# Optimization experiments

Hardware: AMD Instinct MI355X
Metric: run time of the kernel (lower is better)

The kernel has to match this reference:

```python
import jax, jax.numpy as jnp
import numpy as np

B, N, K = 16, 16384, 32

def _fit_motion_svd_batch(pc1, pc2, m):
    # pc1, pc2: (BK, N, 3); m: (BK, N) soft weights
    w_sum = jnp.sum(m, axis=1, keepdims=True)                      # (BK,1)
    pc1_mean = jnp.einsum('bnd,bn->bd', pc1, m) / w_sum            # (BK,3)
    pc2_mean = jnp.einsum('bnd,bn->bd', pc2, m) / w_sum
    pc1_c = pc1 - pc1_mean[:, None, :]
    pc2_c = pc2 - pc2_mean[:, None, :]
    # S = pc1_c^T diag(m) pc2_c : (BK,3,3)
    S = jnp.einsum('bnd,bn,bne->bde', pc1_c, m, pc2_c)
    invalid = jnp.any(jnp.isnan(S), axis=(1, 2))                   # (BK,)
    S_safe = jnp.where(invalid[:, None, None], jnp.eye(3, dtype=S.dtype), S)
    u, s, vh = jnp.linalg.svd(S_safe, full_matrices=True)
    v = jnp.swapaxes(vh, -1, -2)
    R0 = jnp.einsum('bij,bkj->bik', v, u)                          # v @ u^T
    det = jnp.linalg.det(R0)
    diag = jnp.stack([jnp.ones_like(det), jnp.ones_like(det), det], axis=-1)
    R = jnp.einsum('bij,bj,bkj->bik', v, diag, u)                  # v diag u^T
    t = pc2_mean - jnp.einsum('bij,bj->bi', R, pc1_mean)
    R = jnp.where(invalid[:, None, None], jnp.eye(3, dtype=R.dtype), R)
    t = jnp.where(invalid[:, None], jnp.zeros_like(t), t)
    return R, t

def setup_inputs() -> dict:
    key = jax.random.key(0)
    k1, k2, k3 = jax.random.split(key, 3)
    pc = jax.random.normal(k1, (B, N, 3), dtype=jnp.float32)
    mask = jax.random.uniform(k2, (B, N, K), dtype=jnp.float32)
    flow = jax.random.normal(k3, (B, N, 3), dtype=jnp.float32)
    return {"pc": pc, "mask": mask, "flow": flow}

def reference(pc, mask, flow):
    loss_norm = 2
    n_batch, n_point, n_object = mask.shape
    pc2 = pc + flow                                                # (B,N,3)
    m = jnp.swapaxes(mask, 1, 2).reshape(n_batch * n_object, n_point)
    pc_rep = jnp.broadcast_to(pc[:, None], (n_batch, n_object, n_point, 3)).reshape(-1, n_point, 3)
    pc2_rep = jnp.broadcast_to(pc2[:, None], (n_batch, n_object, n_point, 3)).reshape(-1, n_point, 3)
    # pc_transformed is detached in the original; detach inputs to the fit (equivalent)
    R, t = _fit_motion_svd_batch(jax.lax.stop_gradient(pc_rep),
                                 jax.lax.stop_gradient(pc2_rep),
                                 jax.lax.stop_gradient(m))
    pc_tr = jnp.einsum('bij,bnj->bni', R, jax.lax.stop_gradient(pc_rep)) + t[:, None, :]
    pc_tr = pc_tr.reshape(n_batch, n_object, n_point, 3)           # already grad-free
    m4 = m.reshape(n_batch, n_object, n_point)[..., None]          # (B,K,N,1), carries grad
    pc_blend = jnp.sum(m4 * pc_tr, axis=1)                         # (B,N,3)
    diff = pc_blend - pc2
    loss = jnp.linalg.norm(diff, ord=loss_norm, axis=-1)
    return jnp.mean(loss)
```

## Files before the change

kernel.cpp:

```cpp
#include <hip/hip_runtime.h>
#include <math.h>

#define BB 16
#define NPTS 16384
#define KK 32

#define CHUNK1 128
#define NCHUNK1 (NPTS / CHUNK1)

__global__ __launch_bounds__(256) void phase1_kernel(
    const float* __restrict__ pc, const float* __restrict__ mask,
    const float* __restrict__ flow, float* __restrict__ p1) {
  const int b = blockIdx.y;
  const int chunk = blockIdx.x;
  const int tid = threadIdx.x;
  const int plane = tid >> 5;

  const float* pcb = pc + (size_t)b * NPTS * 3;
  const float* flb = flow + (size_t)b * NPTS * 3;
  const size_t mbase = ((size_t)b * NPTS + (size_t)chunk * CHUNK1) * KK;

  float w = 0.f;
  float ax = 0.f, ay = 0.f, az = 0.f;
  float bx = 0.f, by = 0.f, bz = 0.f;
  float M00 = 0.f, M01 = 0.f, M02 = 0.f;
  float M10 = 0.f, M11 = 0.f, M12 = 0.f;
  float M20 = 0.f, M21 = 0.f, M22 = 0.f;

  const int base_p = chunk * CHUNK1 + plane;
#pragma unroll
  for (int i = 0; i < CHUNK1 / 8; ++i) {
    const int p = base_p + i * 8;
    const float m = mask[mbase + (size_t)i * 256 + tid];
    const float px = pcb[p * 3 + 0];
    const float py = pcb[p * 3 + 1];
    const float pz = pcb[p * 3 + 2];
    const float qx = px + flb[p * 3 + 0];
    const float qy = py + flb[p * 3 + 1];
    const float qz = pz + flb[p * 3 + 2];
    w += m;
    const float mx = m * px, my = m * py, mz = m * pz;
    ax += mx; ay += my; az += mz;
    bx = fmaf(m, qx, bx); by = fmaf(m, qy, by); bz = fmaf(m, qz, bz);
    M00 = fmaf(mx, qx, M00); M01 = fmaf(mx, qy, M01); M02 = fmaf(mx, qz, M02);
    M10 = fmaf(my, qx, M10); M11 = fmaf(my, qy, M11); M12 = fmaf(my, qz, M12);
    M20 = fmaf(mz, qx, M20); M21 = fmaf(mz, qy, M21); M22 = fmaf(mz, qz, M22);
  }

  __shared__ float red[256][17];
  red[tid][0] = w;
  red[tid][1] = ax; red[tid][2] = ay; red[tid][3] = az;
  red[tid][4] = bx; red[tid][5] = by; red[tid][6] = bz;
  red[tid][7] = M00; red[tid][8] = M01; red[tid][9] = M02;
  red[tid][10] = M10; red[tid][11] = M11; red[tid][12] = M12;
  red[tid][13] = M20; red[tid][14] = M21; red[tid][15] = M22;
  __syncthreads();

  if (tid < 32) {
    float s[16];
#pragma unroll
    for (int v = 0; v < 16; ++v) s[v] = 0.f;
#pragma unroll
    for (int pl = 0; pl < 8; ++pl) {
#pragma unroll
      for (int v = 0; v < 16; ++v) s[v] += red[pl * 32 + tid][v];
    }
    float* dst = p1 + (((size_t)b * NCHUNK1 + chunk) * 32 + tid) * 16;
#pragma unroll
    for (int v = 0; v < 16; ++v) dst[v] = s[v];
  }
}

__global__ __launch_bounds__(256) void reduce_kernel(
    const float* __restrict__ p1, float* __restrict__ smom) {
  const int idx = blockIdx.x * 256 + threadIdx.x;
  const int b = idx >> 9;
  const int rem = idx & 511;
  const float* src = p1 + (size_t)b * NCHUNK1 * 512 + rem;
  double acc = 0.0;
#pragma unroll 8
  for (int c = 0; c < NCHUNK1; ++c) acc += (double)src[(size_t)c * 512];
  smom[idx] = (float)acc;
}

__global__ void phase2_kernel(const float* __restrict__ smom,
                              float* __restrict__ rt) {
  const int idx = blockIdx.x * blockDim.x + threadIdx.x;
  if (idx >= BB * KK) return;

  double s[16];
#pragma unroll
  for (int v = 0; v < 16; ++v) s[v] = (double)smom[idx * 16 + v];

  const double w = s[0];
  const double mu1[3] = {s[1] / w, s[2] / w, s[3] / w};
  const double bs[3] = {s[4], s[5], s[6]};
  const double mu2[3] = {bs[0] / w, bs[1] / w, bs[2] / w};

  double S[3][3];
#pragma unroll
  for (int d = 0; d < 3; ++d)
#pragma unroll
    for (int e = 0; e < 3; ++e) S[d][e] = s[7 + d * 3 + e] - mu1[d] * bs[e];

  double A[3][3];
#pragma unroll
  for (int i = 0; i < 3; ++i)
#pragma unroll
    for (int j = 0; j < 3; ++j)
      A[i][j] = S[0][i] * S[0][j] + S[1][i] * S[1][j] + S[2][i] * S[2][j];

  double V[3][3] = {{1, 0, 0}, {0, 1, 0}, {0, 0, 1}};

  for (int sweep = 0; sweep < 8; ++sweep) {
#pragma unroll
    for (int pair = 0; pair < 3; ++pair) {
      const int p = (pair == 0) ? 0 : (pair == 1) ? 0 : 1;
      const int q = (pair == 0) ? 1 : (pair == 1) ? 2 : 2;
      const double apq = A[p][q];
      if (fabs(apq) < 1e-300) continue;
      const double app = A[p][p], aqq = A[q][q];
      const double tau = (aqq - app) / (2.0 * apq);
      const double tt =
          ((tau >= 0.0) ? 1.0 : -1.0) / (fabs(tau) + sqrt(1.0 + tau * tau));
      const double c = 1.0 / sqrt(1.0 + tt * tt);
      const double sn = tt * c;
      const int r = 3 - p - q;
      const double arp = A[r][p], arq = A[r][q];
      A[r][p] = A[p][r] = c * arp - sn * arq;
      A[r][q] = A[q][r] = sn * arp + c * arq;
      A[p][p] = app - tt * apq;
      A[q][q] = aqq + tt * apq;
      A[p][q] = A[q][p] = 0.0;
#pragma unroll
      for (int i = 0; i < 3; ++i) {
        const double vip = V[i][p], viq = V[i][q];
        V[i][p] = c * vip - sn * viq;
        V[i][q] = sn * vip + c * viq;
      }
    }
  }

  int id0 = 0, id1 = 1, id2 = 2;
  double lam[3] = {A[0][0], A[1][1], A[2][2]};
  if (lam[id0] < lam[id1]) { int t = id0; id0 = id1; id1 = t; }
  if (lam[id0] < lam[id2]) { int t = id0; id0 = id2; id2 = t; }
  if (lam[id1] < lam[id2]) { int t = id1; id1 = id2; id2 = t; }
  const int ord[3] = {id0, id1, id2};

  double Vs[3][3], U[3][3];
#pragma unroll
  for (int j = 0; j < 3; ++j) {
    const int cj = ord[j];
    const double lj = lam[cj] > 0.0 ? lam[cj] : 0.0;
    const double sig = sqrt(lj);
    const double inv = 1.0 / (sig > 1e-30 ? sig : 1e-30);
#pragma unroll
    for (int i = 0; i < 3; ++i) Vs[i][j] = V[i][cj];
#pragma unroll
    for (int i = 0; i < 3; ++i)
      U[i][j] =
          (S[i][0] * Vs[0][j] + S[i][1] * Vs[1][j] + S[i][2] * Vs[2][j]) * inv;
  }

  const double detS = S[0][0] * (S[1][1] * S[2][2] - S[1][2] * S[2][1]) -
                      S[0][1] * (S[1][0] * S[2][2] - S[1][2] * S[2][0]) +
                      S[0][2] * (S[1][0] * S[2][1] - S[1][1] * S[2][0]);
  const double sgn = (detS >= 0.0) ? 1.0 : -1.0;

  double R[3][3];
#pragma unroll
  for (int i = 0; i < 3; ++i)
#pragma unroll
    for (int j = 0; j < 3; ++j)
      R[i][j] = Vs[i][0] * U[j][0] + Vs[i][1] * U[j][1] + sgn * Vs[i][2] * U[j][2];

  double tv[3];
#pragma unroll
  for (int i = 0; i < 3; ++i)
    tv[i] = mu2[i] - (R[i][0] * mu1[0] + R[i][1] * mu1[1] + R[i][2] * mu1[2]);

  float* dst = rt + (size_t)idx * 12;
#pragma unroll
  for (int i = 0; i < 3; ++i)
#pragma unroll
    for (int j = 0; j < 3; ++j) dst[i * 3 + j] = (float)R[i][j];
#pragma unroll
  for (int i = 0; i < 3; ++i) dst[9 + i] = (float)tv[i];
}

#define PTS3 256
#define NCHUNK3 (NPTS / PTS3)

__global__ __launch_bounds__(256) void phase3_kernel(
    const float* __restrict__ pc, const float* __restrict__ mask,
    const float* __restrict__ flow, const float* __restrict__ rt,
    float* __restrict__ p3) {
  const int b = blockIdx.y;
  const int chunk = blockIdx.x;
  const int tid = threadIdx.x;

  __shared__ float4 sR[KK * 3];
  for (int l = tid; l < KK * 3; l += 256)
    sR[l] = ((const float4*)rt)[(size_t)b * KK * 3 + l];
  __syncthreads();

  const int p = chunk * PTS3 + tid;
  const float4* mrow = (const float4*)(mask + ((size_t)b * NPTS + p) * KK);
  float4 mv[8];
#pragma unroll
  for (int j = 0; j < 8; ++j) mv[j] = mrow[j];

  const float* pcp = pc + ((size_t)b * NPTS + p) * 3;
  const float* flp = flow + ((size_t)b * NPTS + p) * 3;
  const float px = pcp[0], py = pcp[1], pz = pcp[2];

  float C[12];
#pragma unroll
  for (int v = 0; v < 12; ++v) C[v] = 0.f;

#pragma unroll
  for (int k = 0; k < KK; ++k) {
    const float m = ((const float*)&mv[k >> 2])[k & 3];
    const float4 r0 = sR[k * 3 + 0];
    const float4 r1 = sR[k * 3 + 1];
    const float4 r2 = sR[k * 3 + 2];
    C[0] = fmaf(m, r0.x, C[0]); C[1] = fmaf(m, r0.y, C[1]);
    C[2] = fmaf(m, r0.z, C[2]); C[3] = fmaf(m, r0.w, C[3]);
    C[4] = fmaf(m, r1.x, C[4]); C[5] = fmaf(m, r1.y, C[5]);
    C[6] = fmaf(m, r1.z, C[6]); C[7] = fmaf(m, r1.w, C[7]);
    C[8] = fmaf(m, r2.x, C[8]); C[9] = fmaf(m, r2.y, C[9]);
    C[10] = fmaf(m, r2.z, C[10]); C[11] = fmaf(m, r2.w, C[11]);
  }

  const float vx = fmaf(C[0], px, fmaf(C[1], py, fmaf(C[2], pz, C[9])));
  const float vy = fmaf(C[3], px, fmaf(C[4], py, fmaf(C[5], pz, C[10])));
  const float vz = fmaf(C[6], px, fmaf(C[7], py, fmaf(C[8], pz, C[11])));

  const float qx = px + flp[0];
  const float qy = py + flp[1];
  const float qz = pz + flp[2];
  const float dx = vx - qx, dy = vy - qy, dz = vz - qz;
  float acc = sqrtf(dx * dx + dy * dy + dz * dz);

#pragma unroll
  for (int off = 32; off >= 1; off >>= 1) acc += __shfl_xor(acc, off, 64);
  __shared__ float sred[4];
  if ((tid & 63) == 0) sred[tid >> 6] = acc;
  __syncthreads();
  if (tid == 0)
    p3[(size_t)b * NCHUNK3 + chunk] = sred[0] + sred[1] + sred[2] + sred[3];
}

__global__ void phase4_kernel(const float* __restrict__ p3,
                              float* __restrict__ out) {
  const int tid = threadIdx.x;
  float v = 0.f;
#pragma unroll
  for (int j = 0; j < 4; ++j) v += p3[j * 256 + tid];
#pragma unroll
  for (int off = 32; off >= 1; off >>= 1) v += __shfl_xor(v, off, 64);
  __shared__ float sr[4];
  if ((tid & 63) == 0) sr[tid >> 6] = v;
  __syncthreads();
  if (tid == 0)
    out[0] = (sr[0] + sr[1] + sr[2] + sr[3]) * (1.0f / ((float)BB * NPTS));
}

extern "C" void kernel_launch(void* const* d_in, const int* in_sizes, int n_in,
                              void* d_out, int out_size, void* d_ws,
                              size_t ws_size, hipStream_t stream) {
  const float* pc = (const float*)d_in[0];
  const float* mask = (const float*)d_in[1];
  const float* flow = (const float*)d_in[2];
  float* out = (float*)d_out;
  float* ws = (float*)d_ws;

  float* rt = ws;
  float* p1 = ws + 6144;
  float* smom = p1 + (size_t)BB * NCHUNK1 * 512;
  float* p3 = smom + 8192;

  phase1_kernel<<<dim3(NCHUNK1, BB), 256, 0, stream>>>(pc, mask, flow, p1);
  reduce_kernel<<<32, 256, 0, stream>>>(p1, smom);
  phase2_kernel<<<2, 256, 0, stream>>>(smom, rt);
  phase3_kernel<<<dim3(NCHUNK3, BB), 256, 0, stream>>>(pc, mask, flow, rt, p3);
  phase4_kernel<<<1, 256, 0, stream>>>(p3, out);
}
```

Measured before the change: 116.9 us.

## Fuse reduce and SVD solve, fold final reduction into phase3 via atomic ticket

Phase1 now stages each chunk's pc and flow points into shared memory with float4 loads instead of strided scalar global loads. The separate reduce and phase2 kernels are merged into one per-batch solve kernel that keeps the double-precision moment sums in shared memory. The phase4 kernel is removed: the last phase3 block, picked by an atomic ticket counter, performs the final mean reduction. This cuts two kernel launches and their global round-trips, at the cost of a counter reset inside solve_kernel and fence/atomic ordering that correctness now depends on.

```diff
diff --git a/kernel.cpp b/kernel.cpp
--- a/kernel.cpp
+++ b/kernel.cpp
@@ -16,8 +16,18 @@
   const int tid = threadIdx.x;
   const int plane = tid >> 5;
 
-  const float* pcb = pc + (size_t)b * NPTS * 3;
-  const float* flb = flow + (size_t)b * NPTS * 3;
+  __shared__ float spc[CHUNK1 * 3];
+  __shared__ float sfl[CHUNK1 * 3];
+  {
+    const float4* pc4 = (const float4*)(pc + ((size_t)b * NPTS + (size_t)chunk * CHUNK1) * 3);
+    const float4* fl4 = (const float4*)(flow + ((size_t)b * NPTS + (size_t)chunk * CHUNK1) * 3);
+    if (tid < CHUNK1 * 3 / 4) {
+      ((float4*)spc)[tid] = pc4[tid];
+      ((float4*)sfl)[tid] = fl4[tid];
+    }
+  }
+  __syncthreads();
+
   const size_t mbase = ((size_t)b * NPTS + (size_t)chunk * CHUNK1) * KK;
 
   float w = 0.f;
@@ -27,17 +37,16 @@
   float M10 = 0.f, M11 = 0.f, M12 = 0.f;
   float M20 = 0.f, M21 = 0.f, M22 = 0.f;
 
-  const int base_p = chunk * CHUNK1 + plane;
 #pragma unroll
   for (int i = 0; i < CHUNK1 / 8; ++i) {
-    const int p = base_p + i * 8;
+    const int pl = (i * 8 + plane) * 3;
     const float m = mask[mbase + (size_t)i * 256 + tid];
-    const float px = pcb[p * 3 + 0];
-    const float py = pcb[p * 3 + 1];
-    const float pz = pcb[p * 3 + 2];
-    const float qx = px + flb[p * 3 + 0];
-    const float qy = py + flb[p * 3 + 1];
-    const float qz = pz + flb[p * 3 + 2];
+    const float px = spc[pl + 0];
+    const float py = spc[pl + 1];
+    const float pz = spc[pl + 2];
+    const float qx = px + sfl[pl + 0];
+    const float qy = py + sfl[pl + 1];
+    const float qz = pz + sfl[pl + 2];
     w += m;
     const float mx = m * px, my = m * py, mz = m * pz;
     ax += mx; ay += my; az += mz;
@@ -71,131 +80,136 @@
   }
 }
 
-__global__ __launch_bounds__(256) void reduce_kernel(
-    const float* __restrict__ p1, float* __restrict__ smom) {
-  const int idx = blockIdx.x * 256 + threadIdx.x;
-  const int b = idx >> 9;
-  const int rem = idx & 511;
-  const float* src = p1 + (size_t)b * NCHUNK1 * 512 + rem;
+__global__ __launch_bounds__(512) void solve_kernel(
+    const float* __restrict__ p1, float* __restrict__ rt,
+    unsigned int* __restrict__ counter) {
+  const int b = blockIdx.x;
+  const int tid = threadIdx.x;
+
+  if (b == 0 && tid == 0) *counter = 0u;
+
+  const float* src = p1 + (size_t)b * (NCHUNK1 * 512) + tid;
   double acc = 0.0;
 #pragma unroll 8
   for (int c = 0; c < NCHUNK1; ++c) acc += (double)src[(size_t)c * 512];
-  smom[idx] = (float)acc;
-}
-
-__global__ void phase2_kernel(const float* __restrict__ smom,
-                              float* __restrict__ rt) {
-  const int idx = blockIdx.x * blockDim.x + threadIdx.x;
-  if (idx >= BB * KK) return;
-
-  double s[16];
-#pragma unroll
-  for (int v = 0; v < 16; ++v) s[v] = (double)smom[idx * 16 + v];
-
-  const double w = s[0];
-  const double mu1[3] = {s[1] / w, s[2] / w, s[3] / w};
-  const double bs[3] = {s[4], s[5], s[6]};
-  const double mu2[3] = {bs[0] / w, bs[1] / w, bs[2] / w};
-
-  double S[3][3];
-#pragma unroll
-  for (int d = 0; d < 3; ++d)
-#pragma unroll
-    for (int e = 0; e < 3; ++e) S[d][e] = s[7 + d * 3 + e] - mu1[d] * bs[e];
-
-  double A[3][3];
-#pragma unroll
-  for (int i = 0; i < 3; ++i)
-#pragma unroll
-    for (int j = 0; j < 3; ++j)
-      A[i][j] = S[0][i] * S[0][j] + S[1][i] * S[1][j] + S[2][i] * S[2][j];
-
-  double V[3][3] = {{1, 0, 0}, {0, 1, 0}, {0, 0, 1}};
-
-  for (int sweep = 0; sweep < 8; ++sweep) {
-#pragma unroll
-    for (int pair = 0; pair < 3; ++pair) {
-      const int p = (pair == 0) ? 0 : (pair == 1) ? 0 : 1;
-      const int q = (pair == 0) ? 1 : (pair == 1) ? 2 : 2;
-      const double apq = A[p][q];
-      if (fabs(apq) < 1e-300) continue;
-      const double app = A[p][p], aqq = A[q][q];
-      const double tau = (aqq - app) / (2.0 * apq);
-      const double tt =
-          ((tau >= 0.0) ? 1.0 : -1.0) / (fabs(tau) + sqrt(1.0 + tau * tau));
-      const double c = 1.0 / sqrt(1.0 + tt * tt);
-      const double sn = tt * c;
-      const int r = 3 - p - q;
-      const double arp = A[r][p], arq = A[r][q];
-      A[r][p] = A[p][r] = c * arp - sn * arq;
-      A[r][q] = A[q][r] = sn * arp + c * arq;
-      A[p][p] = app - tt * apq;
-      A[q][q] = aqq + tt * apq;
-      A[p][q] = A[q][p] = 0.0;
-#pragma unroll
-      for (int i = 0; i < 3; ++i) {
-        const double vip = V[i][p], viq = V[i][q];
-        V[i][p] = c * vip - sn * viq;
-        V[i][q] = sn * vip + c * viq;
+  __shared__ double smom[512];
+  smom[tid] = acc;
+  __syncthreads();
+
+  if (tid < 32) {
+    const int k = tid;
+    double s[16];
+#pragma unroll
+    for (int v = 0; v < 16; ++v) s[v] = smom[k * 16 + v];
+
+    const double w = s[0];
+    const double mu1[3] = {s[1] / w, s[2] / w, s[3] / w};
+    const double bs[3] = {s[4], s[5], s[6]};
+    const double mu2[3] = {bs[0] / w, bs[1] / w, bs[2] / w};
+
+    double S[3][3];
+#pragma unroll
+    for (int d = 0; d < 3; ++d)
+#pragma unroll
+      for (int e = 0; e < 3; ++e) S[d][e] = s[7 + d * 3 + e] - mu1[d] * bs[e];
+
+    double A[3][3];
+#pragma unroll
+    for (int i = 0; i < 3; ++i)
+#pragma unroll
+      for (int j = 0; j < 3; ++j)
+        A[i][j] = S[0][i] * S[0][j] + S[1][i] * S[1][j] + S[2][i] * S[2][j];
+
+    double V[3][3] = {{1, 0, 0}, {0, 1, 0}, {0, 0, 1}};
+
+    for (int sweep = 0; sweep < 8; ++sweep) {
+#pragma unroll
+      for (int pair = 0; pair < 3; ++pair) {
+        const int p = (pair == 0) ? 0 : (pair == 1) ? 0 : 1;
+        const int q = (pair == 0) ? 1 : (pair == 1) ? 2 : 2;
+        const double apq = A[p][q];
+        if (fabs(apq) < 1e-300) continue;
+        const double app = A[p][p], aqq = A[q][q];
+        const double tau = (aqq - app) / (2.0 * apq);
+        const double tt =
+            ((tau >= 0.0) ? 1.0 : -1.0) / (fabs(tau) + sqrt(1.0 + tau * tau));
+        const double c = 1.0 / sqrt(1.0 + tt * tt);
+        const double sn = tt * c;
+        const int r = 3 - p - q;
+        const double arp = A[r][p], arq = A[r][q];
+        A[r][p] = A[p][r] = c * arp - sn * arq;
+        A[r][q] = A[q][r] = sn * arp + c * arq;
+        A[p][p] = app - tt * apq;
+        A[q][q] = aqq + tt * apq;
+        A[p][q] = A[q][p] = 0.0;
+#pragma unroll
+        for (int i = 0; i < 3; ++i) {
+          const double vip = V[i][p], viq = V[i][q];
+          V[i][p] = c * vip - sn * viq;
+          V[i][q] = sn * vip + c * viq;
+        }
       }
     }
-  }
-
-  int id0 = 0, id1 = 1, id2 = 2;
-  double lam[3] = {A[0][0], A[1][1], A[2][2]};
-  if (lam[id0] < lam[id1]) { int t = id0; id0 = id1; id1 = t; }
-  if (lam[id0] < lam[id2]) { int t = id0; id0 = id2; id2 = t; }
-  if (lam[id1] < lam[id2]) { int t = id1; id1 = id2; id2 = t; }
-  const int ord[3] = {id0, id1, id2};
-
-  double Vs[3][3], U[3][3];
-#pragma unroll
-  for (int j = 0; j < 3; ++j) {
-    const int cj = ord[j];
-    const double lj = lam[cj] > 0.0 ? lam[cj] : 0.0;
-    const double sig = sqrt(lj);
-    const double inv = 1.0 / (sig > 1e-30 ? sig : 1e-30);
-#pragma unroll
-    for (int i = 0; i < 3; ++i) Vs[i][j] = V[i][cj];
+
+    int id0 = 0, id1 = 1, id2 = 2;
+    double lam[3] = {A[0][0], A[1][1], A[2][2]};
+    if (lam[id0] < lam[id1]) { int t = id0; id0 = id1; id1 = t; }
+    if (lam[id0] < lam[id2]) { int t = id0; id0 = id2; id2 = t; }
+    if (lam[id1] < lam[id2]) { int t = id1; id1 = id2; id2 = t; }
+    const int ord[3] = {id0, id1, id2};
+
+    double Vs[3][3], U[3][3];
+#pragma unroll
+    for (int j = 0; j < 3; ++j) {
+      const int cj = ord[j];
+      const double lj = lam[cj] > 0.0 ? lam[cj] : 0.0;
+      const double sig = sqrt(lj);
+      const double inv = 1.0 / (sig > 1e-30 ? sig : 1e-30);
+#pragma unroll
+      for (int i = 0; i < 3; ++i) Vs[i][j] = V[i][cj];
+#pragma unroll
+      for (int i = 0; i < 3; ++i)
+        U[i][j] =
+            (S[i][0] * Vs[0][j] + S[i][1] * Vs[1][j] + S[i][2] * Vs[2][j]) * inv;
+    }
+
+    const double detS = S[0][0] * (S[1][1] * S[2][2] - S[1][2] * S[2][1]) -
+                        S[0][1] * (S[1][0] * S[2][2] - S[1][2] * S[2][0]) +
+                        S[0][2] * (S[1][0] * S[2][1] - S[1][1] * S[2][0]);
+    const double sgn = (detS >= 0.0) ? 1.0 : -1.0;
+
+    double R[3][3];
 #pragma unroll
     for (int i = 0; i < 3; ++i)
-      U[i][j] =
-          (S[i][0] * Vs[0][j] + S[i][1] * Vs[1][j] + S[i][2] * Vs[2][j]) * inv;
-  }
-
-  const double detS = S[0][0] * (S[1][1] * S[2][2] - S[1][2] * S[2][1]) -
-                      S[0][1] * (S[1][0] * S[2][2] - S[1][2] * S[2][0]) +
-                      S[0][2] * (S[1][0] * S[2][1] - S[1][1] * S[2][0]);
-  const double sgn = (detS >= 0.0) ? 1.0 : -1.0;
-
-  double R[3][3];
-#pragma unroll
-  for (int i = 0; i < 3; ++i)
-#pragma unroll
-    for (int j = 0; j < 3; ++j)
-      R[i][j] = Vs[i][0] * U[j][0] + Vs[i][1] * U[j][1] + sgn * Vs[i][2] * U[j][2];
-
-  double tv[3];
-#pragma unroll
-  for (int i = 0; i < 3; ++i)
-    tv[i] = mu2[i] - (R[i][0] * mu1[0] + R[i][1] * mu1[1] + R[i][2] * mu1[2]);
-
-  float* dst = rt + (size_t)idx * 12;
-#pragma unroll
-  for (int i = 0; i < 3; ++i)
-#pragma unroll
-    for (int j = 0; j < 3; ++j) dst[i * 3 + j] = (float)R[i][j];
-#pragma unroll
-  for (int i = 0; i < 3; ++i) dst[9 + i] = (float)tv[i];
+#pragma unroll
+      for (int j = 0; j < 3; ++j)
+        R[i][j] =
+            Vs[i][0] * U[j][0] + Vs[i][1] * U[j][1] + sgn * Vs[i][2] * U[j][2];
+
+    double tv[3];
+#pragma unroll
+    for (int i = 0; i < 3; ++i)
+      tv[i] = mu2[i] - (R[i][0] * mu1[0] + R[i][1] * mu1[1] + R[i][2] * mu1[2]);
+
+    float* dst = rt + ((size_t)b * KK + k) * 12;
+#pragma unroll
+    for (int i = 0; i < 3; ++i)
+#pragma unroll
+      for (int j = 0; j < 3; ++j) dst[i * 3 + j] = (float)R[i][j];
+#pragma unroll
+    for (int i = 0; i < 3; ++i) dst[9 + i] = (float)tv[i];
+  }
 }
 
 #define PTS3 256
 #define NCHUNK3 (NPTS / PTS3)
+#define NBLK3 (NCHUNK3 * BB)
 
 __global__ __launch_bounds__(256) void phase3_kernel(
     const float* __restrict__ pc, const float* __restrict__ mask,
     const float* __restrict__ flow, const float* __restrict__ rt,
-    float* __restrict__ p3) {
+    float* __restrict__ p3, unsigned int* __restrict__ counter,
+    float* __restrict__ out) {
   const int b = blockIdx.y;
   const int chunk = blockIdx.x;
   const int tid = threadIdx.x;
@@ -248,23 +262,28 @@
   __shared__ float sred[4];
   if ((tid & 63) == 0) sred[tid >> 6] = acc;
   __syncthreads();
-  if (tid == 0)
+
+  __shared__ unsigned int sticket;
+  if (tid == 0) {
     p3[(size_t)b * NCHUNK3 + chunk] = sred[0] + sred[1] + sred[2] + sred[3];
-}
-
-__global__ void phase4_kernel(const float* __restrict__ p3,
-                              float* __restrict__ out) {
-  const int tid = threadIdx.x;
-  float v = 0.f;
-#pragma unroll
-  for (int j = 0; j < 4; ++j) v += p3[j * 256 + tid];
-#pragma unroll
-  for (int off = 32; off >= 1; off >>= 1) v += __shfl_xor(v, off, 64);
-  __shared__ float sr[4];
-  if ((tid & 63) == 0) sr[tid >> 6] = v;
-  __syncthreads();
-  if (tid == 0)
-    out[0] = (sr[0] + sr[1] + sr[2] + sr[3]) * (1.0f / ((float)BB * NPTS));
+    __threadfence();
+    sticket = atomicAdd(counter, 1u);
+  }
+  __syncthreads();
+
+  if (sticket == NBLK3 - 1) {
+    __threadfence();
+    float v = 0.f;
+#pragma unroll
+    for (int j = 0; j < 4; ++j) v += p3[j * 256 + tid];
+#pragma unroll
+    for (int off = 32; off >= 1; off >>= 1) v += __shfl_xor(v, off, 64);
+    __shared__ float sr[4];
+    if ((tid & 63) == 0) sr[tid >> 6] = v;
+    __syncthreads();
+    if (tid == 0)
+      out[0] = (sr[0] + sr[1] + sr[2] + sr[3]) * (1.0f / ((float)BB * NPTS));
+  }
 }
 
 extern "C" void kernel_launch(void* const* d_in, const int* in_sizes, int n_in,
@@ -278,12 +297,11 @@
 
   float* rt = ws;
   float* p1 = ws + 6144;
-  float* smom = p1 + (size_t)BB * NCHUNK1 * 512;
-  float* p3 = smom + 8192;
+  float* p3 = p1 + (size_t)BB * NCHUNK1 * 512;
+  unsigned int* counter = (unsigned int*)(p3 + 1024);
 
   phase1_kernel<<<dim3(NCHUNK1, BB), 256, 0, stream>>>(pc, mask, flow, p1);
-  reduce_kernel<<<32, 256, 0, stream>>>(p1, smom);
-  phase2_kernel<<<2, 256, 0, stream>>>(smom, rt);
-  phase3_kernel<<<dim3(NCHUNK3, BB), 256, 0, stream>>>(pc, mask, flow, rt, p3);
-  phase4_kernel<<<1, 256, 0, stream>>>(p3, out);
+  solve_kernel<<<BB, 512, 0, stream>>>(p1, rt, counter);
+  phase3_kernel<<<dim3(NCHUNK3, BB), 256, 0, stream>>>(pc, mask, flow, rt, p3,
+                                                       counter, out);
 }
```

Measured after the change: 133.4 us. 1.14x slower.
